# Kernel tuning notes

Measured on AMD Instinct MI355X. Metric: run time of the kernel, lower is better.

## Reference

```python
import jax, jax.numpy as jnp
import numpy as np

NUM_HEADS = 16
HEAD_DIM = 64  # hidden_size // num_heads = 1024 // 16


def setup_inputs() -> dict:
    key = jax.random.key(0)
    ks = jax.random.split(key, 5)
    B, S, D = 4, 2048, 1024
    scale = 1.0 / np.sqrt(D)
    return {
        "hidden_states": jax.random.normal(ks[0], (B, S, D), dtype=jnp.float32),
        "Wq": jax.random.normal(ks[1], (D, D), dtype=jnp.float32) * scale,
        "Wk": jax.random.normal(ks[2], (D, D), dtype=jnp.float32) * scale,
        "Wv": jax.random.normal(ks[3], (D, D), dtype=jnp.float32) * scale,
        "Wo": jax.random.normal(ks[4], (D, D), dtype=jnp.float32) * scale,
    }


def reference(hidden_states, Wq, Wk, Wv, Wo):
    B, S, D = hidden_states.shape
    H, hd = NUM_HEADS, HEAD_DIM
    # torch nn.Linear(y = x @ W.T), bias=False
    q = (hidden_states @ Wq.T).reshape(B, S, H, hd)
    k = (hidden_states @ Wk.T).reshape(B, S, H, hd)
    v = (hidden_states @ Wv.T).reshape(B, S, H, hd)
    q = q / jnp.sqrt(jnp.float32(hd))
    # scores: [B, H, S, S] — module materializes full score matrix
    scores = jnp.einsum("bqhd,bkhd->bhqk", q, k)
    weights = jax.nn.softmax(scores, axis=-1)
    attn = jnp.einsum("bhqk,bkhd->bqhd", weights, v).reshape(B, S, D)
    return attn @ Wo.T
```

## Files before the change

### kernel.cpp

```cpp
#include <hip/hip_runtime.h>

using u16 = unsigned short;
using u32 = unsigned int;
typedef __attribute__((ext_vector_type(8))) short bf16x8;
typedef __attribute__((ext_vector_type(4))) short bf16x4;
typedef __attribute__((ext_vector_type(4))) float f32x4;
typedef __attribute__((ext_vector_type(16))) float f32x16;
typedef __attribute__((ext_vector_type(4))) u32 u32x4;

__device__ __forceinline__ u16 f2bf(float f) {
  u32 u = __builtin_bit_cast(u32, f);
  u += 0x7FFFu + ((u >> 16) & 1u);
  return (u16)(u >> 16);
}

__device__ __forceinline__ void load_lds16(const void* g, void* l) {
  typedef const __attribute__((address_space(1))) u32 GA;
  typedef __attribute__((address_space(3))) u32 LA;
  __builtin_amdgcn_global_load_lds((GA*)g, (LA*)l, 16, 0, 0);
}

__device__ __forceinline__ bf16x4 tr16(const u16* p) {
  typedef __attribute__((address_space(3))) const u16 LT;
  bf16x4 d;
  asm volatile("ds_read_b64_tr_b16 %0, %1" : "=v"(d) : "v"((LT*)p));
  return d;
}

__device__ __forceinline__ float exp2_fast(float x) {
  float r;
  asm("v_exp_f32 %0, %1" : "=v"(r) : "v"(x));
  return r;
}

__device__ __forceinline__ u32 cvt_pk_bf16(float lo, float hi) {
  u32 r;
  asm("v_cvt_pk_bf16_f32 %0, %1, %2" : "=v"(r) : "v"(lo), "v"(hi));
  return r;
}

__device__ __forceinline__ void permlane32_swap(u32& a, u32& b) {
  asm volatile("v_permlane32_swap_b32 %0, %1" : "+v"(a), "+v"(b));
}

__global__ void cvt_bf16(const float* __restrict__ src, u16* __restrict__ dst,
                         int n4, float scale) {
  int i = blockIdx.x * blockDim.x + threadIdx.x;
  if (i >= n4) return;
  float4 v = reinterpret_cast<const float4*>(src)[i];
  ushort4 o;
  o.x = f2bf(v.x * scale);
  o.y = f2bf(v.y * scale);
  o.z = f2bf(v.z * scale);
  o.w = f2bf(v.w * scale);
  reinterpret_cast<ushort4*>(dst)[i] = o;
}

template <typename OutT>
__global__ __launch_bounds__(256, 2) void gemm_bt(
    const u16* __restrict__ A, const u16* __restrict__ Bw,
    OutT* __restrict__ C, int M, int N, int K) {
  __shared__ u16 At[128 * 32];
  __shared__ u16 Bt[128 * 32];
  const int tid = threadIdx.x;
  const int wid = tid >> 6, lane = tid & 63;
  const int wr = wid >> 1, wc = wid & 1;
  const int laneR = lane & 15, laneG = lane >> 4;
  const int laneK = laneG * 8;

  const int nbm = M >> 7;
  const int nwg = gridDim.x;
  const int cpx = nwg >> 3;
  const int id = blockIdx.x;
  const int swz = (id & 7) * cpx + (id >> 3);
  const int bm = swz % nbm, bn = swz / nbm;

  f32x4 acc[4][4];
#pragma unroll
  for (int i = 0; i < 4; ++i)
#pragma unroll
    for (int j = 0; j < 4; ++j) acc[i][j] = f32x4{0.f, 0.f, 0.f, 0.f};

  const int e0 = tid * 8;
  const int r0 = e0 >> 5, c0 = e0 & 31;
  const u16* Ab = A + (size_t)(bm * 128) * K;
  const u16* Bb = Bw + (size_t)(bn * 128) * K;

  for (int k0 = 0; k0 < K; k0 += 32) {
#pragma unroll
    for (int i = 0; i < 2; ++i) {
      load_lds16(Ab + (size_t)(i * 64 + r0) * K + k0 + c0, &At[(i * 256 + wid * 64) * 8]);
      load_lds16(Bb + (size_t)(i * 64 + r0) * K + k0 + c0, &Bt[(i * 256 + wid * 64) * 8]);
    }
    __syncthreads();
    bf16x8 af[4], bfr[4];
#pragma unroll
    for (int i = 0; i < 4; ++i)
      af[i] = *(const bf16x8*)&At[(wr * 64 + i * 16 + laneR) * 32 + laneK];
#pragma unroll
    for (int j = 0; j < 4; ++j)
      bfr[j] = *(const bf16x8*)&Bt[(wc * 64 + j * 16 + laneR) * 32 + laneK];
#pragma unroll
    for (int i = 0; i < 4; ++i)
#pragma unroll
      for (int j = 0; j < 4; ++j)
        acc[i][j] = __builtin_amdgcn_mfma_f32_16x16x32_bf16(af[i], bfr[j], acc[i][j], 0, 0, 0);
    __syncthreads();
  }

  const int crow = bm * 128 + wr * 64;
  const int ccol = bn * 128 + wc * 64;
#pragma unroll
  for (int i = 0; i < 4; ++i)
#pragma unroll
    for (int j = 0; j < 4; ++j)
#pragma unroll
      for (int r = 0; r < 4; ++r) {
        int row = crow + i * 16 + laneG * 4 + r;
        int col = ccol + j * 16 + laneR;
        float v = acc[i][j][r];
        if constexpr (sizeof(OutT) == 2)
          C[(size_t)row * N + col] = f2bf(v);
        else
          C[(size_t)row * N + col] = v;
      }
}

__global__ __launch_bounds__(512, 4) void flash_attn(
    const u16* __restrict__ QKV, u16* __restrict__ O) {
  constexpr int S = 2048, DQ = 3072, DO = 1024;
  __shared__ u16 Kt[2][4096];
  __shared__ u16 Vt[2][4096];
  const int tid = threadIdx.x, wid = tid >> 6, lane = tid & 63;
  const int lq = lane & 31, hi = lane >> 5;
  const int qt = blockIdx.x;
  const int b = blockIdx.y >> 4, h = blockIdx.y & 15;

  const size_t bq = (size_t)b * S * DQ;
  const u16* Qg = QKV + bq + h * 64;
  const u16* Kg = QKV + bq + 1024 + h * 64;
  const u16* Vg = QKV + bq + 2048 + h * 64;
  const int qrow0 = qt * 256 + wid * 32;

  const int k_kv = tid >> 3;
  const int k_col = ((tid & 7) ^ (k_kv & 7)) * 8;
  const int v_kv = ((tid >> 5) << 2) | ((tid >> 1) & 3);
  const int v_hd = (((tid >> 3) & 3) << 4) | ((tid & 1) << 3);

  bf16x8 qf[4];
#pragma unroll
  for (int kc = 0; kc < 4; ++kc)
    qf[kc] = *(const bf16x8*)&Qg[(size_t)(qrow0 + lq) * DQ + kc * 16 + hi * 8];

  f32x16 o0, o1;
#pragma unroll
  for (int r = 0; r < 16; ++r) { o0[r] = 0.f; o1[r] = 0.f; }
  float l = 0.f;

  auto stage = [&](int buf, int kv0) {
    load_lds16(Kg + (size_t)(kv0 + k_kv) * DQ + k_col, &Kt[buf][wid * 512]);
    load_lds16(Vg + (size_t)(kv0 + v_kv) * DQ + v_hd, &Vt[buf][wid * 512]);
  };

  stage(0, 0);
  __syncthreads();

  for (int t = 0; t < 32; ++t) {
    const int cur = t & 1;
    stage(cur ^ 1, ((t + 1) & 31) * 64);

    f32x16 st[2];
#pragma unroll
    for (int blk = 0; blk < 2; ++blk) {
#pragma unroll
      for (int r = 0; r < 16; ++r) st[blk][r] = 0.f;
      bf16x8 kf[4];
#pragma unroll
      for (int kc = 0; kc < 4; ++kc) {
        int kv = blk * 32 + lq;
        int byt = kv * 128 + ((kc * 32 + hi * 16) ^ ((kv & 7) << 4));
        kf[kc] = *(const bf16x8*)((const char*)&Kt[cur][0] + byt);
      }
      __builtin_amdgcn_s_setprio(1);
#pragma unroll
      for (int kc = 0; kc < 4; ++kc)
        st[blk] = __builtin_amdgcn_mfma_f32_32x32x16_bf16(kf[kc], qf[kc], st[blk], 0, 0, 0);
      __builtin_amdgcn_s_setprio(0);
    }

    float ps = 0.f;
#pragma unroll
    for (int blk = 0; blk < 2; ++blk)
#pragma unroll
      for (int r = 0; r < 16; ++r) {
        float p = exp2_fast(st[blk][r]);
        st[blk][r] = p;
        ps += p;
      }
    l += ps;

    u32 W0[8], W1[8];
#pragma unroll
    for (int r2 = 0; r2 < 8; ++r2) {
      W0[r2] = cvt_pk_bf16(st[0][2 * r2], st[0][2 * r2 + 1]);
      W1[r2] = cvt_pk_bf16(st[1][2 * r2], st[1][2 * r2 + 1]);
    }
    bf16x8 pb[4];
#pragma unroll
    for (int ks = 0; ks < 2; ++ks) {
      u32 a0 = W0[4 * ks], a2 = W0[4 * ks + 2];
      u32 a1 = W0[4 * ks + 1], a3 = W0[4 * ks + 3];
      permlane32_swap(a0, a2);
      permlane32_swap(a1, a3);
      pb[ks] = __builtin_bit_cast(bf16x8, u32x4{a0, a1, a2, a3});
    }
#pragma unroll
    for (int ks = 0; ks < 2; ++ks) {
      u32 a0 = W1[4 * ks], a2 = W1[4 * ks + 2];
      u32 a1 = W1[4 * ks + 1], a3 = W1[4 * ks + 3];
      permlane32_swap(a0, a2);
      permlane32_swap(a1, a3);
      pb[2 + ks] = __builtin_bit_cast(bf16x8, u32x4{a0, a1, a2, a3});
    }

#pragma unroll
    for (int c2 = 0; c2 < 2; ++c2) {
      bf16x4 vh[4][2];
      const int hb = c2 * 2 + ((lane >> 4) & 1);
#pragma unroll
      for (int ks = 0; ks < 4; ++ks)
#pragma unroll
        for (int p2 = 0; p2 < 2; ++p2) {
          int a = ks * 4 + hi * 2 + p2;
          vh[ks][p2] = tr16(&Vt[cur][(a * 4 + hb) * 64 + (lane & 15) * 4]);
        }
      asm volatile("s_waitcnt lgkmcnt(0)" ::: "memory");
      __builtin_amdgcn_sched_barrier(0);
      __builtin_amdgcn_s_setprio(1);
      f32x16 oc = c2 ? o1 : o0;
#pragma unroll
      for (int ks = 0; ks < 4; ++ks) {
        bf16x8 vf = __builtin_shufflevector(vh[ks][0], vh[ks][1], 0, 1, 2, 3, 4, 5, 6, 7);
        oc = __builtin_amdgcn_mfma_f32_32x32x16_bf16(vf, pb[ks], oc, 0, 0, 0);
      }
      if (c2) o1 = oc; else o0 = oc;
      __builtin_amdgcn_s_setprio(0);
    }

    __syncthreads();
  }

  l += __shfl_xor(l, 32);
  const float inv = 1.0f / l;
  const size_t boo = (size_t)b * S * DO + h * 64;
  const size_t qb = boo + (size_t)(qrow0 + lq) * DO;
#pragma unroll
  for (int r = 0; r < 16; ++r) {
    int hd = (r & 3) + 8 * (r >> 2) + 4 * hi;
    O[qb + hd] = f2bf(o0[r] * inv);
    O[qb + 32 + hd] = f2bf(o1[r] * inv);
  }
}

extern "C" void kernel_launch(void* const* d_in, const int* in_sizes, int n_in,
                              void* d_out, int out_size, void* d_ws, size_t ws_size,
                              hipStream_t stream) {
  const float* hs = (const float*)d_in[0];
  const float* Wq = (const float*)d_in[1];
  const float* Wk = (const float*)d_in[2];
  const float* Wv = (const float*)d_in[3];
  const float* Wo = (const float*)d_in[4];
  float* out = (float*)d_out;

  constexpr int Bn = 4, S = 2048, Dm = 1024;
  constexpr int M = Bn * S;
  constexpr size_t SZ = (size_t)M * Dm;
  constexpr size_t WSZ = (size_t)Dm * Dm;

  u16* wsp = (u16*)d_ws;
  u16* QKVb = wsp;
  u16* hs16 = QKVb + (size_t)M * 3072;
  u16* Ob = hs16;
  u16* W16 = hs16 + SZ;
  u16* Wo16 = W16 + 3 * WSZ;
  (void)ws_size; (void)in_sizes; (void)n_in; (void)out_size;

  cvt_bf16<<<(int)(SZ / 4 / 256), 256, 0, stream>>>(hs, hs16, (int)(SZ / 4), 1.0f);
  cvt_bf16<<<(int)(WSZ / 4 / 256), 256, 0, stream>>>(Wq, W16, (int)(WSZ / 4), 0.125f * 1.44269504f);
  cvt_bf16<<<(int)(WSZ / 4 / 256), 256, 0, stream>>>(Wk, W16 + WSZ, (int)(WSZ / 4), 1.0f);
  cvt_bf16<<<(int)(WSZ / 4 / 256), 256, 0, stream>>>(Wv, W16 + 2 * WSZ, (int)(WSZ / 4), 1.0f);
  cvt_bf16<<<(int)(WSZ / 4 / 256), 256, 0, stream>>>(Wo, Wo16, (int)(WSZ / 4), 1.0f);

  gemm_bt<u16><<<(M / 128) * (3072 / 128), 256, 0, stream>>>(hs16, W16, QKVb, M, 3072, Dm);

  flash_attn<<<dim3(S / 256, Bn * 16), 512, 0, stream>>>(QKVb, Ob);

  gemm_bt<float><<<(M / 128) * (Dm / 128), 256, 0, stream>>>(Ob, Wo16, out, M, Dm, Dm);
}
```

Before: 208.9 us.

## Replace QKV projection GEMM with 256x256 tiled, LDS-pipelined 8-wave kernel

Adds a new gemm256 kernel with 256x256 output tiles, 8 waves, 64-wide K tiles staged via direct global-to-LDS loads into a swizzled double buffer, and an interleaved schedule of half-tile stages with MFMA quads and raised wave priority. The QKV projection now uses it instead of the 128x128 gemm_bt. The goal is more operand reuse per LDS byte and overlap of global loads with MFMA work. The trade-off is 128KB LDS per block, fewer blocks in flight (192), many barriers, and hand-written waitcnt counts that must match the load order.

```diff
diff --git a/kernel.cpp b/kernel.cpp
--- a/kernel.cpp
+++ b/kernel.cpp
@@ -69,8 +69,7 @@
   const int laneK = laneG * 8;
 
   const int nbm = M >> 7;
-  const int nwg = gridDim.x;
-  const int cpx = nwg >> 3;
+  const int cpx = gridDim.x >> 3;
   const int id = blockIdx.x;
   const int swz = (id & 7) * cpx + (id >> 3);
   const int bm = swz % nbm, bn = swz / nbm;
@@ -126,6 +125,151 @@
       }
 }
 
+template <int MH, int NH>
+__device__ __forceinline__ void mfma_quad(f32x4 (&acc)[8][4], bf16x8 (&afr)[4][2],
+                                          bf16x8 (&bfr)[2][2]) {
+  __builtin_amdgcn_s_setprio(1);
+#pragma unroll
+  for (int m = 0; m < 4; ++m)
+#pragma unroll
+    for (int n = 0; n < 2; ++n)
+#pragma unroll
+      for (int ks = 0; ks < 2; ++ks)
+        acc[MH * 4 + m][NH * 2 + n] = __builtin_amdgcn_mfma_f32_16x16x32_bf16(
+            afr[m][ks], bfr[n][ks], acc[MH * 4 + m][NH * 2 + n], 0, 0, 0);
+  __builtin_amdgcn_s_setprio(0);
+}
+
+#define GBAR() __builtin_amdgcn_s_barrier()
+#define WAITL()                                            \
+  do {                                                     \
+    asm volatile("s_waitcnt lgkmcnt(0)" ::: "memory");     \
+    __builtin_amdgcn_sched_barrier(0);                     \
+  } while (0)
+#define WAITLV()                                                    \
+  do {                                                              \
+    asm volatile("s_waitcnt vmcnt(2) lgkmcnt(0)" ::: "memory");     \
+    __builtin_amdgcn_sched_barrier(0);                              \
+  } while (0)
+
+template <typename OutT>
+__global__ __launch_bounds__(512, 2) void gemm256(
+    const u16* __restrict__ A, const u16* __restrict__ Bw,
+    OutT* __restrict__ C, int M, int N, int K) {
+  __shared__ __align__(16) char ldsb[131072];
+  const int tid = threadIdx.x;
+  const int wid = tid >> 6, lane = tid & 63;
+  const int wr = wid >> 2, wc = wid & 3;
+  const int laneR = lane & 15, laneG = lane >> 4;
+  const int swzR = (laneR & 7) << 4;
+
+  const int nbm = M >> 8;
+  const int cpx = gridDim.x >> 3;
+  const int id = blockIdx.x;
+  const int swzid = (id & 7) * cpx + (id >> 3);
+  const int bm = swzid % nbm, bn = swzid / nbm;
+
+  const u16* Ab = A + (size_t)(bm * 256) * K;
+  const u16* Bb = Bw + (size_t)(bn * 256) * K;
+
+  const int s_r = tid >> 3;
+  const int s_k = ((tid & 7) ^ (s_r & 7)) * 8;
+
+  auto stage_half = [&](const u16* Xb, int regio, int buf, int hh, int kt) {
+    char* d = ldsb + regio + buf * 32768 + hh * 16384 + wid * 1024;
+#pragma unroll
+    for (int j = 0; j < 2; ++j)
+      load_lds16(Xb + (size_t)(hh * 128 + j * 64 + s_r) * K + kt * 64 + s_k,
+                 d + j * 8192);
+  };
+  auto rdA = [&](int buf, int mh, int m, int ks) -> bf16x8 {
+    return *(const bf16x8*)(ldsb + buf * 32768 + wr * 16384 +
+                            (mh * 64 + m * 16 + laneR) * 128 +
+                            ((ks * 64 + laneG * 16) ^ swzR));
+  };
+  auto rdB = [&](int buf, int nh, int n, int ks) -> bf16x8 {
+    return *(const bf16x8*)(ldsb + 65536 + buf * 32768 + (wc >> 1) * 16384 +
+                            ((wc & 1) * 64 + nh * 32 + n * 16 + laneR) * 128 +
+                            ((ks * 64 + laneG * 16) ^ swzR));
+  };
+
+  f32x4 acc[8][4];
+#pragma unroll
+  for (int i = 0; i < 8; ++i)
+#pragma unroll
+    for (int j = 0; j < 4; ++j) acc[i][j] = f32x4{0.f, 0.f, 0.f, 0.f};
+
+  bf16x8 afr[4][2], bfr[2][2];
+  auto readAB = [&](int buf, int mh, int nh) {
+#pragma unroll
+    for (int m = 0; m < 4; ++m) {
+      afr[m][0] = rdA(buf, mh, m, 0);
+      afr[m][1] = rdA(buf, mh, m, 1);
+    }
+#pragma unroll
+    for (int n = 0; n < 2; ++n) {
+      bfr[n][0] = rdB(buf, nh, n, 0);
+      bfr[n][1] = rdB(buf, nh, n, 1);
+    }
+  };
+  auto readB = [&](int buf, int nh) {
+#pragma unroll
+    for (int n = 0; n < 2; ++n) {
+      bfr[n][0] = rdB(buf, nh, n, 0);
+      bfr[n][1] = rdB(buf, nh, n, 1);
+    }
+  };
+
+  const int NT = K >> 6, NI = K >> 7;
+
+  stage_half(Ab, 0, 0, 0, 0);
+  stage_half(Ab, 0, 0, 1, 0);
+  stage_half(Bb, 65536, 0, 0, 0);
+  stage_half(Bb, 65536, 0, 1, 0);
+  stage_half(Ab, 0, 1, 0, 1);
+  asm volatile("s_waitcnt vmcnt(2)" ::: "memory");
+  GBAR();
+
+  for (int i = 0; i < NI; ++i) {
+    const int t1 = (2 * i + 1) & (NT - 1);
+    const int t2 = (2 * i + 2) & (NT - 1);
+    const int t3 = (2 * i + 3) & (NT - 1);
+    readAB(0, 0, 0); stage_half(Ab, 0, 1, 1, t1); WAITL(); GBAR();
+    mfma_quad<0, 0>(acc, afr, bfr); GBAR();
+    readB(0, 1); stage_half(Bb, 65536, 1, 0, t1); WAITL(); GBAR();
+    mfma_quad<0, 1>(acc, afr, bfr); GBAR();
+    readAB(0, 1, 0); stage_half(Bb, 65536, 1, 1, t1); WAITL(); GBAR();
+    mfma_quad<1, 0>(acc, afr, bfr); GBAR();
+    readB(0, 1); stage_half(Ab, 0, 0, 0, t2); WAITLV(); GBAR();
+    mfma_quad<1, 1>(acc, afr, bfr); GBAR();
+    readAB(1, 0, 0); stage_half(Ab, 0, 0, 1, t2); WAITL(); GBAR();
+    mfma_quad<0, 0>(acc, afr, bfr); GBAR();
+    readB(1, 1); stage_half(Bb, 65536, 0, 0, t2); WAITL(); GBAR();
+    mfma_quad<0, 1>(acc, afr, bfr); GBAR();
+    readAB(1, 1, 0); stage_half(Bb, 65536, 0, 1, t2); WAITL(); GBAR();
+    mfma_quad<1, 0>(acc, afr, bfr); GBAR();
+    readB(1, 1); stage_half(Ab, 0, 1, 0, t3); WAITLV(); GBAR();
+    mfma_quad<1, 1>(acc, afr, bfr); GBAR();
+  }
+
+  const int crow = bm * 256 + wr * 128;
+  const int ccol = bn * 256 + wc * 64;
+#pragma unroll
+  for (int mf = 0; mf < 8; ++mf)
+#pragma unroll
+    for (int nf = 0; nf < 4; ++nf)
+#pragma unroll
+      for (int r = 0; r < 4; ++r) {
+        int row = crow + mf * 16 + laneG * 4 + r;
+        int col = ccol + nf * 16 + laneR;
+        float v = acc[mf][nf][r];
+        if constexpr (sizeof(OutT) == 2)
+          C[(size_t)row * N + col] = f2bf(v);
+        else
+          C[(size_t)row * N + col] = v;
+      }
+}
+
 __global__ __launch_bounds__(512, 4) void flash_attn(
     const u16* __restrict__ QKV, u16* __restrict__ O) {
   constexpr int S = 2048, DQ = 3072, DO = 1024;
@@ -291,7 +435,7 @@
   cvt_bf16<<<(int)(WSZ / 4 / 256), 256, 0, stream>>>(Wv, W16 + 2 * WSZ, (int)(WSZ / 4), 1.0f);
   cvt_bf16<<<(int)(WSZ / 4 / 256), 256, 0, stream>>>(Wo, Wo16, (int)(WSZ / 4), 1.0f);
 
-  gemm_bt<u16><<<(M / 128) * (3072 / 128), 256, 0, stream>>>(hs16, W16, QKVb, M, 3072, Dm);
+  gemm256<u16><<<(M / 256) * (3072 / 256), 512, 0, stream>>>(hs16, W16, QKVb, M, 3072, Dm);
 
   flash_attn<<<dim3(S / 256, Bn * 16), 512, 0, stream>>>(QKVb, Ob);
 
```

Result: faster. 204.1 us (-2.3%).
